# Kernel tuning notes

Hardware: AMD Instinct MI355X
Metric: run time of the kernel (lower is better)

The kernel has to match this reference:

```python
import jax, jax.numpy as jnp
import numpy as np

B = 8192      # batch
C = 4096      # in_channels
K = 5         # group_size (odd, centered window)


def setup_inputs() -> dict:
    key = jax.random.key(0)
    kx, kw, kb = jax.random.split(key, 3)
    x = jax.random.normal(kx, (B, C), dtype=jnp.float32)
    # Banded weights: W[i, k] multiplies x[:, i + k - K//2] (zero outside range).
    W = jax.random.normal(kw, (C, K), dtype=jnp.float32) * 0.1
    b = jax.random.normal(kb, (C,), dtype=jnp.float32) * 0.1
    return {"x": x, "W": W, "b": b}


def reference(x, W, b):
    # out[:, i] = sum_k W[i, k] * x[:, i + k - K//2] + b[i]
    # Boundary clipping in the original == zero padding here.
    Bn, Cn = x.shape
    Kn = W.shape[1]
    half = Kn // 2
    xp = jnp.pad(x, ((0, 0), (half, half)))  # [B, C + K - 1]
    acc = jnp.zeros_like(x)
    for k in range(Kn):  # tiny fixed loop (K=5), fused shift-multiply-add
        acc = acc + xp[:, k:k + Cn] * W[:, k]
    return acc + b
```

## Files before the change

kernel.cpp:

```cpp
#include <hip/hip_runtime.h>


#define B_ROWS 8192
#define C_CH   4096
#define KWIN   5
#define ROWS_PER_BLOCK 16

__global__ __launch_bounds__(256) void grouped_linear_kernel(
    const float* __restrict__ x, const float* __restrict__ W,
    const float* __restrict__ bias, float* __restrict__ out)
{
    const int chunk = (blockIdx.x << 8) + threadIdx.x;
    const int c     = chunk << 2;
    const int r0    = blockIdx.y * ROWS_PER_BLOCK;

    const float4* W4 = (const float4*)(W + (size_t)c * KWIN);
    const float4 w0 = W4[0];
    const float4 w1 = W4[1];
    const float4 w2 = W4[2];
    const float4 w3 = W4[3];
    const float4 w4 = W4[4];
    const float4 bv = ((const float4*)bias)[chunk];

    const bool has_m = (c > 0);
    const bool has_p = (c + 4 < C_CH);
    const float4 zero = make_float4(0.f, 0.f, 0.f, 0.f);

    const float4* xrow = (const float4*)(x   + (size_t)r0 * C_CH);
    float4*       orow = (float4*)      (out + (size_t)r0 * C_CH);

    #pragma unroll 2
    for (int r = 0; r < ROWS_PER_BLOCK; ++r) {
        const float4 xm = has_m ? xrow[chunk - 1] : zero;
        const float4 xc = xrow[chunk];
        const float4 xp = has_p ? xrow[chunk + 1] : zero;

        const float win0 = xm.z, win1 = xm.w;
        const float win2 = xc.x, win3 = xc.y, win4 = xc.z, win5 = xc.w;
        const float win6 = xp.x, win7 = xp.y;

        float4 o;
        o.x = fmaf(w0.x, win0, fmaf(w0.y, win1, fmaf(w0.z, win2, fmaf(w0.w, win3, fmaf(w1.x, win4, bv.x)))));
        o.y = fmaf(w1.y, win1, fmaf(w1.z, win2, fmaf(w1.w, win3, fmaf(w2.x, win4, fmaf(w2.y, win5, bv.y)))));
        o.z = fmaf(w2.z, win2, fmaf(w2.w, win3, fmaf(w3.x, win4, fmaf(w3.y, win5, fmaf(w3.z, win6, bv.z)))));
        o.w = fmaf(w3.w, win3, fmaf(w4.x, win4, fmaf(w4.y, win5, fmaf(w4.z, win6, fmaf(w4.w, win7, bv.w)))));

        orow[chunk] = o;
        xrow += C_CH / 4;
        orow += C_CH / 4;
    }
}

extern "C" void kernel_launch(void* const* d_in, const int* in_sizes, int n_in,
                              void* d_out, int out_size, void* d_ws, size_t ws_size,
                              hipStream_t stream) {
    const float* x    = (const float*)d_in[0];
    const float* W    = (const float*)d_in[1];
    const float* bias = (const float*)d_in[2];
    float* out = (float*)d_out;

    dim3 grid(C_CH / 4 / 256, B_ROWS / ROWS_PER_BLOCK);
    dim3 block(256);
    grouped_linear_kernel<<<grid, block, 0, stream>>>(x, W, bias, out);
}
```

Measured before the change: 249.6 us.

## Replace neighbor float4 loads with wave shuffles, halo loads, and double-buffered prefetch

```diff
diff --git a/kernel.cpp b/kernel.cpp
--- a/kernel.cpp
+++ b/kernel.cpp
@@ -3,18 +3,47 @@
 
 #define B_ROWS 8192
 #define C_CH   4096
-#define KWIN   5
-#define ROWS_PER_BLOCK 16
+#define NR     8
+#define ROWB   (C_CH * 4)
 
-__global__ __launch_bounds__(256) void grouped_linear_kernel(
+typedef unsigned int u32;
+typedef u32 u32x4 __attribute__((ext_vector_type(4)));
+typedef float f4 __attribute__((ext_vector_type(4)));
+typedef float f2 __attribute__((ext_vector_type(2)));
+
+__device__ __forceinline__ u32x4 make_srd(const void* p, u32 bytes) {
+    union { const void* p; u32 w[2]; } u; u.p = p;
+    u32x4 d; d.x = u.w[0]; d.y = u.w[1]; d.z = bytes; d.w = 0x00020000u;
+    return d;
+}
+__device__ __forceinline__ f4 bl4(u32x4 s, u32 voff, u32 soff) {
+    f4 r;
+    asm volatile("buffer_load_dwordx4 %0, %1, %2, %3 offen"
+                 : "=&v"(r) : "v"(voff), "s"(s), "s"(soff) : "memory");
+    return r;
+}
+__device__ __forceinline__ f2 bl2(u32x4 s, u32 voff, u32 soff) {
+    f2 r;
+    asm volatile("buffer_load_dwordx2 %0, %1, %2, %3 offen"
+                 : "=&v"(r) : "v"(voff), "s"(s), "s"(soff) : "memory");
+    return r;
+}
+__device__ __forceinline__ void bs4(u32x4 s, u32 voff, u32 soff, f4 v) {
+    asm volatile("buffer_store_dwordx4 %0, %1, %2, %3 offen"
+                 :: "v"(v), "v"(voff), "s"(s), "s"(soff) : "memory");
+}
+
+__global__ __launch_bounds__(256, 8) void grouped_linear_kernel(
     const float* __restrict__ x, const float* __restrict__ W,
     const float* __restrict__ bias, float* __restrict__ out)
 {
-    const int chunk = (blockIdx.x << 8) + threadIdx.x;
+    const int tid   = threadIdx.x;
+    const int chunk = (blockIdx.x << 8) + tid;
     const int c     = chunk << 2;
-    const int r0    = blockIdx.y * ROWS_PER_BLOCK;
+    const int lane  = tid & 63;
+    const int r0    = blockIdx.y * NR;
 
-    const float4* W4 = (const float4*)(W + (size_t)c * KWIN);
+    const float4* W4 = (const float4*)(W + (size_t)c * 5);
     const float4 w0 = W4[0];
     const float4 w1 = W4[1];
     const float4 w2 = W4[2];
@@ -22,32 +51,55 @@
     const float4 w4 = W4[4];
     const float4 bv = ((const float4*)bias)[chunk];
 
-    const bool has_m = (c > 0);
-    const bool has_p = (c + 4 < C_CH);
-    const float4 zero = make_float4(0.f, 0.f, 0.f, 0.f);
+    const u32x4 sx = make_srd(x,   (u32)B_ROWS * ROWB);
+    const u32x4 so = make_srd(out, (u32)B_ROWS * ROWB);
 
-    const float4* xrow = (const float4*)(x   + (size_t)r0 * C_CH);
-    float4*       orow = (float4*)      (out + (size_t)r0 * C_CH);
+    const u32 cvoff = (u32)chunk * 16u;
+    const u32 hvoff = (lane == 63) ? (cvoff + 16u)
+                                   : (u32)((int)cvoff - lane * 16 - 8);
+    const u32 sbase = (u32)r0 * (u32)ROWB;
 
-    #pragma unroll 2
-    for (int r = 0; r < ROWS_PER_BLOCK; ++r) {
-        const float4 xm = has_m ? xrow[chunk - 1] : zero;
-        const float4 xc = xrow[chunk];
-        const float4 xp = has_p ? xrow[chunk + 1] : zero;
+    const bool has_m = (chunk > 0);
+    const bool has_p = (chunk < 1023);
 
-        const float win0 = xm.z, win1 = xm.w;
+    f4 bc[2]; f2 hb[2];
+    bc[0] = bl4(sx, cvoff, sbase);
+    hb[0] = bl2(sx, hvoff, sbase);
+
+    #pragma unroll
+    for (int r = 0; r < NR; ++r) {
+        const int cur = r & 1;
+        if (r + 1 < NR) {
+            const u32 snext = sbase + (u32)(r + 1) * ROWB;
+            bc[cur ^ 1] = bl4(sx, cvoff, snext);
+            hb[cur ^ 1] = bl2(sx, hvoff, snext);
+        }
+        if (r == 0)           asm volatile("s_waitcnt vmcnt(2)" ::: "memory");
+        else if (r == NR - 1) asm volatile("s_waitcnt vmcnt(1)" ::: "memory");
+        else                  asm volatile("s_waitcnt vmcnt(3)" ::: "memory");
+        __builtin_amdgcn_sched_barrier(0);
+
+        const f4 xc = bc[cur];
+        const f2 hl = hb[cur];
+
+        const float mz = __shfl_up(xc.z, 1);
+        const float mw = __shfl_up(xc.w, 1);
+        const float px = __shfl_down(xc.x, 1);
+        const float py = __shfl_down(xc.y, 1);
+
+        const float win0 = has_m ? (lane == 0  ? hl.x : mz) : 0.f;
+        const float win1 = has_m ? (lane == 0  ? hl.y : mw) : 0.f;
         const float win2 = xc.x, win3 = xc.y, win4 = xc.z, win5 = xc.w;
-        const float win6 = xp.x, win7 = xp.y;
+        const float win6 = has_p ? (lane == 63 ? hl.x : px) : 0.f;
+        const float win7 = has_p ? (lane == 63 ? hl.y : py) : 0.f;
 
-        float4 o;
+        f4 o;
         o.x = fmaf(w0.x, win0, fmaf(w0.y, win1, fmaf(w0.z, win2, fmaf(w0.w, win3, fmaf(w1.x, win4, bv.x)))));
         o.y = fmaf(w1.y, win1, fmaf(w1.z, win2, fmaf(w1.w, win3, fmaf(w2.x, win4, fmaf(w2.y, win5, bv.y)))));
         o.z = fmaf(w2.z, win2, fmaf(w2.w, win3, fmaf(w3.x, win4, fmaf(w3.y, win5, fmaf(w3.z, win6, bv.z)))));
         o.w = fmaf(w3.w, win3, fmaf(w4.x, win4, fmaf(w4.y, win5, fmaf(w4.z, win6, fmaf(w4.w, win7, bv.w)))));
 
-        orow[chunk] = o;
-        xrow += C_CH / 4;
-        orow += C_CH / 4;
+        bs4(so, cvoff, sbase + (u32)r * ROWB, o);
     }
 }
 
@@ -59,7 +111,7 @@
     const float* bias = (const float*)d_in[2];
     float* out = (float*)d_out;
 
-    dim3 grid(C_CH / 4 / 256, B_ROWS / ROWS_PER_BLOCK);
+    dim3 grid(C_CH / 4 / 256, B_ROWS / NR);
     dim3 block(256);
     grouped_linear_kernel<<<grid, block, 0, stream>>>(x, W, bias, out);
 }
```

New measurement: 238.4 us. -4.5%, faster.
